# Kernel optimization log

Measured on AMD Instinct MI355X. Metric: run time of the kernel, lower is better.

The kernel has to match this reference:

```python
import jax, jax.numpy as jnp
import numpy as np

NUM_BLOCKS = 2
RES_LAYERS = 10
HID = 128
IN_CH = 256
MID_CH = 512
OUT_CH = 256
DILATIONS = [2 ** l for b in range(NUM_BLOCKS) for l in range(RES_LAYERS)]
GOOD = sum(DILATIONS)  # 2046
NLAYERS = NUM_BLOCKS * RES_LAYERS


def setup_inputs() -> dict:
    key = jax.random.key(0)
    ks = jax.random.split(key, 16)
    s = 0.05
    B, T = 8, 8192
    inp = {
        "inputs": jax.random.normal(ks[0], (B, IN_CH, T), dtype=jnp.float32),
        "Wi": jax.random.normal(ks[1], (HID, IN_CH), dtype=jnp.float32) * s,
        "bi": jax.random.normal(ks[2], (HID,), dtype=jnp.float32) * s,
        "Wf": jax.random.normal(ks[3], (NLAYERS, HID, HID, 2), dtype=jnp.float32) * s,
        "bf": jax.random.normal(ks[4], (NLAYERS, HID), dtype=jnp.float32) * s,
        "Wg": jax.random.normal(ks[5], (NLAYERS, HID, HID, 2), dtype=jnp.float32) * s,
        "bg": jax.random.normal(ks[6], (NLAYERS, HID), dtype=jnp.float32) * s,
        "Wr": jax.random.normal(ks[7], (NLAYERS, HID, HID), dtype=jnp.float32) * s,
        "br": jax.random.normal(ks[8], (NLAYERS, HID), dtype=jnp.float32) * s,
        "W1": jax.random.normal(ks[9], (MID_CH, HID), dtype=jnp.float32) * s,
        "b1": jax.random.normal(ks[10], (MID_CH,), dtype=jnp.float32) * s,
        "W2": jax.random.normal(ks[11], (OUT_CH, MID_CH), dtype=jnp.float32) * s,
        "b2": jax.random.normal(ks[12], (OUT_CH,), dtype=jnp.float32) * s,
    }
    return inp


def _dilated_k2(x, W, b, d):
    # x: [B, C, T] -> [B, C, T-d]
    y = jnp.einsum("oi,bit->bot", W[:, :, 0], x[:, :, :-d]) \
        + jnp.einsum("oi,bit->bot", W[:, :, 1], x[:, :, d:])
    return y + b[None, :, None]


def reference(inputs, Wi, bi, Wf, bf, Wg, bg, Wr, br, W1, b1, W2, b2):
    T = inputs.shape[2]
    target = T - GOOD
    res = jnp.einsum("oi,bit->bot", Wi, inputs) + bi[None, :, None]
    final = None
    for idx, d in enumerate(DILATIONS):
        f = jnp.tanh(_dilated_k2(res, Wf[idx], bf[idx], d))
        g = jax.nn.sigmoid(_dilated_k2(res, Wg[idx], bg[idx], d))
        out = f * g
        x = jnp.einsum("oi,bit->bot", Wr[idx], out) + br[idx][None, :, None]
        res = x + res[:, :, d:]
        # NOTE: original code computes split conv then immediately overwrites
        # it with x[:, :, -target:]; the split conv is dead code, so skip it.
        skip = x[:, :, -target:]
        final = skip if final is None else final + skip
    h = jax.nn.relu(final)
    h = jnp.einsum("oi,bit->bot", W1, h) + b1[None, :, None]
    h = jax.nn.relu(h)
    h = jnp.einsum("oi,bit->bot", W2, h) + b2[None, :, None]
    n, c, l = h.shape
    return jnp.transpose(h, (0, 2, 1)).reshape(n * l, c)
```

## Files before the change

kernel.cpp:

```cpp
#include <hip/hip_runtime.h>


#define TT 8192
#define HIDC 128
#define GOODC 2046
#define TGT 6146
#define NL 20

typedef _Float16 half8_t __attribute__((ext_vector_type(8)));
typedef _Float16 half4_t __attribute__((ext_vector_type(4)));
typedef float floatx4 __attribute__((ext_vector_type(4)));

__device__ __forceinline__ floatx4 mfma16(half8_t a, half8_t b, floatx4 c) {
  return __builtin_amdgcn_mfma_f32_16x16x32_f16(a, b, c, 0, 0, 0);
}

__global__ void prep_kernel(const float* __restrict__ Wi, const float* __restrict__ Wf,
                            const float* __restrict__ Wg, const float* __restrict__ Wr,
                            const float* __restrict__ W1, const float* __restrict__ W2,
                            _Float16* __restrict__ WIh, _Float16* __restrict__ WFG,
                            _Float16* __restrict__ WRh, _Float16* __restrict__ W1h,
                            _Float16* __restrict__ W2h) {
  int idx = blockIdx.x * blockDim.x + threadIdx.x;
  int stride = gridDim.x * blockDim.x;
  for (int i = idx; i < NL * 256 * 256; i += stride) {
    int l = i >> 16; int m = (i >> 8) & 255; int k = i & 255;
    int tap = k >> 7; int ci = k & 127;
    float v;
    if (m < 128) v = Wf[(((size_t)l * 128 + m) * 128 + ci) * 2 + tap];
    else         v = Wg[(((size_t)l * 128 + (m - 128)) * 128 + ci) * 2 + tap];
    WFG[i] = (_Float16)v;
  }
  for (int i = idx; i < NL * 128 * 128; i += stride) WRh[i] = (_Float16)Wr[i];
  for (int i = idx; i < 128 * 256; i += stride) WIh[i] = (_Float16)Wi[i];
  for (int i = idx; i < 512 * 128; i += stride) W1h[i] = (_Float16)W1[i];
  for (int i = idx; i < 256 * 512; i += stride) W2h[i] = (_Float16)W2[i];
}

__global__ __launch_bounds__(256, 3) void input_kernel(
    const float* __restrict__ inp, const _Float16* __restrict__ WIh,
    const float* __restrict__ bi, _Float16* __restrict__ R0) {
  __shared__ __align__(16) _Float16 Xs[64][264];
  const int tid = threadIdx.x;
  const int lane = tid & 63;
  const int w = tid >> 6;
  const int ml = lane & 15;
  const int mq = lane >> 4;
  const int b = blockIdx.y;
  const int u0 = blockIdx.x * 64;
  const float* ib = inp + (size_t)b * 256 * TT;

  for (int i = tid; i < 64 * 16; i += 256) {
    int n4 = i & 15;
    int kg = i >> 4;
    const float* src = ib + (size_t)(kg * 4) * TT + u0 + n4 * 4;
    floatx4 c0 = *(const floatx4*)(src);
    floatx4 c1 = *(const floatx4*)(src + TT);
    floatx4 c2 = *(const floatx4*)(src + 2 * TT);
    floatx4 c3 = *(const floatx4*)(src + 3 * TT);
#pragma unroll
    for (int t = 0; t < 4; ++t) {
      half4_t h;
      h[0] = (_Float16)c0[t]; h[1] = (_Float16)c1[t];
      h[2] = (_Float16)c2[t]; h[3] = (_Float16)c3[t];
      *(half4_t*)&Xs[n4 * 4 + t][kg * 4] = h;
    }
  }
  __syncthreads();

  floatx4 acc[2][4];
#pragma unroll
  for (int a = 0; a < 2; ++a)
#pragma unroll
    for (int c = 0; c < 4; ++c) acc[a][c] = floatx4{0.f, 0.f, 0.f, 0.f};

  const _Float16* Aw = WIh + (size_t)(32 * w + ml) * 256;
  for (int kk = 0; kk < 8; ++kk) {
    const int ko = kk * 32 + mq * 8;
    half8_t a0 = *(const half8_t*)(Aw + ko);
    half8_t a1 = *(const half8_t*)(Aw + 16 * 256 + ko);
#pragma unroll
    for (int nt = 0; nt < 4; ++nt) {
      half8_t bv = *(const half8_t*)&Xs[nt * 16 + ml][ko];
      acc[0][nt] = mfma16(a0, bv, acc[0][nt]);
      acc[1][nt] = mfma16(a1, bv, acc[1][nt]);
    }
  }
  __syncthreads();
  float* Xf = (float*)&Xs[0][0];
#pragma unroll
  for (int mt = 0; mt < 2; ++mt) {
    const int mb = 32 * w + mt * 16 + mq * 4;
#pragma unroll
    for (int nt = 0; nt < 4; ++nt)
      *(floatx4*)&Xf[(nt * 16 + ml) * 132 + mb] = acc[mt][nt];
  }
  __syncthreads();
  _Float16* Rb = R0 + (size_t)b * TT * HIDC;
  for (int i = tid; i < 64 * 16; i += 256) {
    int n = i >> 4; int c = i & 15;
    floatx4 x0 = *(const floatx4*)&Xf[n * 132 + c * 8];
    floatx4 x1 = *(const floatx4*)&Xf[n * 132 + c * 8 + 4];
    floatx4 b0 = *(const floatx4*)(bi + c * 8);
    floatx4 b1v = *(const floatx4*)(bi + c * 8 + 4);
    half8_t h;
#pragma unroll
    for (int t = 0; t < 4; ++t) {
      h[t] = (_Float16)(x0[t] + b0[t]);
      h[4 + t] = (_Float16)(x1[t] + b1v[t]);
    }
    *(half8_t*)(Rb + (size_t)(u0 + n) * HIDC + c * 8) = h;
  }
}

__global__ __launch_bounds__(512, 4) void layer_kernel(
    const _Float16* __restrict__ Rin, _Float16* __restrict__ Rout,
    const _Float16* __restrict__ WFG, const _Float16* __restrict__ WR,
    const float* __restrict__ bf, const float* __restrict__ bg,
    const float* __restrict__ br, int d, int ustart) {
  __shared__ __align__(16) _Float16 Xs[128][136];
  __shared__ __align__(16) _Float16 Os[128][136];
  const int tid = threadIdx.x;
  const int lane = tid & 63;
  const int w = tid >> 6;
  const int wm = w & 3;
  const int wn = w >> 2;
  const int ml = lane & 15;
  const int mq = lane >> 4;
  const int b = blockIdx.y;
  const int u0 = ustart + blockIdx.x * 128;
  const _Float16* Rb = Rin + (size_t)b * TT * HIDC;
  _Float16* Ro = Rout + (size_t)b * TT * HIDC;

  floatx4 accF[2][4], accG[2][4];
#pragma unroll
  for (int a = 0; a < 2; ++a)
#pragma unroll
    for (int c = 0; c < 4; ++c) {
      accF[a][c] = floatx4{0.f, 0.f, 0.f, 0.f};
      accG[a][c] = floatx4{0.f, 0.f, 0.f, 0.f};
    }

  for (int p = 0; p < 2; ++p) {
    for (int i = tid; i < 128 * 16; i += 512) {
      int n = i >> 4; int c = i & 15;
      int u = u0 + n - (p ? 0 : d);
      if (u > TT - 1) u = TT - 1;
      *(half8_t*)&Xs[n][c * 8] = *(const half8_t*)(Rb + (size_t)u * HIDC + c * 8);
    }
    __syncthreads();
    const _Float16* Af = WFG + (size_t)(32 * wm + ml) * 256 + p * 128;
    const _Float16* Ag = WFG + (size_t)(128 + 32 * wm + ml) * 256 + p * 128;
    for (int kk = 0; kk < 4; ++kk) {
      const int ko = kk * 32 + mq * 8;
      half8_t aF0 = *(const half8_t*)(Af + ko);
      half8_t aF1 = *(const half8_t*)(Af + 16 * 256 + ko);
      half8_t aG0 = *(const half8_t*)(Ag + ko);
      half8_t aG1 = *(const half8_t*)(Ag + 16 * 256 + ko);
#pragma unroll
      for (int nt = 0; nt < 4; ++nt) {
        half8_t bv = *(const half8_t*)&Xs[wn * 64 + nt * 16 + ml][ko];
        accF[0][nt] = mfma16(aF0, bv, accF[0][nt]);
        accF[1][nt] = mfma16(aF1, bv, accF[1][nt]);
        accG[0][nt] = mfma16(aG0, bv, accG[0][nt]);
        accG[1][nt] = mfma16(aG1, bv, accG[1][nt]);
      }
    }
    __syncthreads();
  }

#pragma unroll
  for (int mt = 0; mt < 2; ++mt) {
    const int mb = 32 * wm + mt * 16 + mq * 4;
    floatx4 bfv = *(const floatx4*)(bf + mb);
    floatx4 bgv = *(const floatx4*)(bg + mb);
#pragma unroll
    for (int nt = 0; nt < 4; ++nt) {
      half4_t o;
#pragma unroll
      for (int r = 0; r < 4; ++r) {
        float fp = accF[mt][nt][r] + bfv[r];
        float gp = accG[mt][nt][r] + bgv[r];
        float fv = 2.0f / (1.0f + __expf(-2.0f * fp)) - 1.0f;
        float gv = 1.0f / (1.0f + __expf(-gp));
        o[r] = (_Float16)(fv * gv);
      }
      *(half4_t*)&Os[wn * 64 + nt * 16 + ml][mb] = o;
    }
  }
  __syncthreads();

  floatx4 accX[2][4];
#pragma unroll
  for (int a = 0; a < 2; ++a)
#pragma unroll
    for (int c = 0; c < 4; ++c) accX[a][c] = floatx4{0.f, 0.f, 0.f, 0.f};
  const _Float16* Ar = WR + (size_t)(32 * wm + ml) * 128;
#pragma unroll
  for (int kk = 0; kk < 4; ++kk) {
    const int ko = kk * 32 + mq * 8;
    half8_t a0 = *(const half8_t*)(Ar + ko);
    half8_t a1 = *(const half8_t*)(Ar + 16 * 128 + ko);
#pragma unroll
    for (int nt = 0; nt < 4; ++nt) {
      half8_t bv = *(const half8_t*)&Os[wn * 64 + nt * 16 + ml][ko];
      accX[0][nt] = mfma16(a0, bv, accX[0][nt]);
      accX[1][nt] = mfma16(a1, bv, accX[1][nt]);
    }
  }
  __syncthreads();

#pragma unroll
  for (int mt = 0; mt < 2; ++mt) {
    const int mb = 32 * wm + mt * 16 + mq * 4;
#pragma unroll
    for (int nt = 0; nt < 4; ++nt) {
      half4_t h;
#pragma unroll
      for (int r = 0; r < 4; ++r) h[r] = (_Float16)accX[mt][nt][r];
      *(half4_t*)&Os[wn * 64 + nt * 16 + ml][mb] = h;
    }
  }
  __syncthreads();

  for (int i = tid; i < 128 * 16; i += 512) {
    int n = i >> 4; int c = i & 15;
    int u = u0 + n;
    if (u < TT) {
      half8_t xv = *(const half8_t*)&Os[n][c * 8];
      half8_t rv = *(const half8_t*)&Xs[n][c * 8];
      floatx4 b0 = *(const floatx4*)(br + c * 8);
      floatx4 b1v = *(const floatx4*)(br + c * 8 + 4);
      half8_t o;
#pragma unroll
      for (int t = 0; t < 4; ++t) {
        o[t] = (_Float16)((float)xv[t] + (float)rv[t] + b0[t]);
        o[4 + t] = (_Float16)((float)xv[4 + t] + (float)rv[4 + t] + b1v[t]);
      }
      *(half8_t*)(Ro + (size_t)u * HIDC + c * 8) = o;
    }
  }
}

__global__ __launch_bounds__(512, 4) void head_kernel(
    const _Float16* __restrict__ Rfin, const _Float16* __restrict__ R0,
    const _Float16* __restrict__ W1h, const _Float16* __restrict__ W2h,
    const float* __restrict__ b1, const float* __restrict__ b2,
    float* __restrict__ out) {
  __shared__ __align__(16) _Float16 Hs[64][136];
  __shared__ __align__(16) _Float16 H1s[64][264];
  const int tid = threadIdx.x;
  const int lane = tid & 63;
  const int w = tid >> 6;
  const int ml = lane & 15;
  const int mq = lane >> 4;
  const int b = blockIdx.y;
  const int u0 = GOODC + blockIdx.x * 64;
  const _Float16* Ra = Rfin + (size_t)b * TT * HIDC;
  const _Float16* Rz = R0 + (size_t)b * TT * HIDC;

  for (int i = tid; i < 64 * 16; i += 512) {
    int n = i >> 4; int c = i & 15;
    int u = u0 + n; if (u > TT - 1) u = TT - 1;
    half8_t a = *(const half8_t*)(Ra + (size_t)u * HIDC + c * 8);
    half8_t z = *(const half8_t*)(Rz + (size_t)u * HIDC + c * 8);
    half8_t h;
#pragma unroll
    for (int t = 0; t < 8; ++t) {
      float v = (float)a[t] - (float)z[t];
      h[t] = (_Float16)(v > 0.f ? v : 0.f);
    }
    *(half8_t*)&Hs[n][c * 8] = h;
  }
  __syncthreads();

  floatx4 acc2[2][4];
#pragma unroll
  for (int a = 0; a < 2; ++a)
#pragma unroll
    for (int c = 0; c < 4; ++c) acc2[a][c] = floatx4{0.f, 0.f, 0.f, 0.f};

  for (int p = 0; p < 2; ++p) {
    floatx4 acc1[2][4];
#pragma unroll
    for (int a = 0; a < 2; ++a)
#pragma unroll
      for (int c = 0; c < 4; ++c) acc1[a][c] = floatx4{0.f, 0.f, 0.f, 0.f};
    const _Float16* A1 = W1h + (size_t)(256 * p + 32 * w + ml) * 128;
#pragma unroll
    for (int kk = 0; kk < 4; ++kk) {
      const int ko = kk * 32 + mq * 8;
      half8_t av0 = *(const half8_t*)(A1 + ko);
      half8_t av1 = *(const half8_t*)(A1 + 16 * 128 + ko);
#pragma unroll
      for (int nt = 0; nt < 4; ++nt) {
        half8_t bv = *(const half8_t*)&Hs[nt * 16 + ml][ko];
        acc1[0][nt] = mfma16(av0, bv, acc1[0][nt]);
        acc1[1][nt] = mfma16(av1, bv, acc1[1][nt]);
      }
    }
    __syncthreads();
#pragma unroll
    for (int mt = 0; mt < 2; ++mt) {
      const int mb = 32 * w + mt * 16 + mq * 4;
      floatx4 bv = *(const floatx4*)(b1 + 256 * p + mb);
#pragma unroll
      for (int nt = 0; nt < 4; ++nt) {
        half4_t h;
#pragma unroll
        for (int r = 0; r < 4; ++r) {
          float v = acc1[mt][nt][r] + bv[r];
          h[r] = (_Float16)(v > 0.f ? v : 0.f);
        }
        *(half4_t*)&H1s[nt * 16 + ml][mb] = h;
      }
    }
    __syncthreads();
    const _Float16* A2 = W2h + (size_t)(32 * w + ml) * 512 + p * 256;
    for (int kk = 0; kk < 8; ++kk) {
      const int ko = kk * 32 + mq * 8;
      half8_t av0 = *(const half8_t*)(A2 + ko);
      half8_t av1 = *(const half8_t*)(A2 + 16 * 512 + ko);
#pragma unroll
      for (int nt = 0; nt < 4; ++nt) {
        half8_t bv = *(const half8_t*)&H1s[nt * 16 + ml][ko];
        acc2[0][nt] = mfma16(av0, bv, acc2[0][nt]);
        acc2[1][nt] = mfma16(av1, bv, acc2[1][nt]);
      }
    }
    __syncthreads();
  }

#pragma unroll
  for (int mt = 0; mt < 2; ++mt) {
    const int mb = 32 * w + mt * 16 + mq * 4;
    floatx4 bv = *(const floatx4*)(b2 + mb);
#pragma unroll
    for (int nt = 0; nt < 4; ++nt) {
      half4_t h;
#pragma unroll
      for (int r = 0; r < 4; ++r) h[r] = (_Float16)(acc2[mt][nt][r] + bv[r]);
      *(half4_t*)&H1s[nt * 16 + ml][mb] = h;
    }
  }
  __syncthreads();
  for (int i = tid; i < 64 * 32; i += 512) {
    int n = i >> 5; int g = i & 31;
    int u = u0 + n;
    if (u < TT) {
      half8_t v = *(const half8_t*)&H1s[n][g * 8];
      float* dst = out + ((size_t)b * TGT + (u - GOODC)) * 256 + g * 8;
      floatx4 v0, v1;
#pragma unroll
      for (int t = 0; t < 4; ++t) { v0[t] = (float)v[t]; v1[t] = (float)v[4 + t]; }
      *(floatx4*)dst = v0;
      *(floatx4*)(dst + 4) = v1;
    }
  }
}

extern "C" void kernel_launch(void* const* d_in, const int* in_sizes, int n_in,
                              void* d_out, int out_size, void* d_ws, size_t ws_size,
                              hipStream_t stream) {
  const float* inputs = (const float*)d_in[0];
  const float* Wi = (const float*)d_in[1];
  const float* bi = (const float*)d_in[2];
  const float* Wf = (const float*)d_in[3];
  const float* bf = (const float*)d_in[4];
  const float* Wg = (const float*)d_in[5];
  const float* bg = (const float*)d_in[6];
  const float* Wr = (const float*)d_in[7];
  const float* br = (const float*)d_in[8];
  const float* W1 = (const float*)d_in[9];
  const float* b1 = (const float*)d_in[10];
  const float* W2 = (const float*)d_in[11];
  const float* b2 = (const float*)d_in[12];
  float* out = (float*)d_out;

  char* ws = (char*)d_ws;
  _Float16* R0h = (_Float16*)(ws + 0);
  _Float16* Ph  = (_Float16*)(ws + 16777216);
  _Float16* Qh  = (_Float16*)(ws + 33554432);
  _Float16* WFG = (_Float16*)(ws + 50331648);
  _Float16* WRh = (_Float16*)(ws + 52953088);
  _Float16* WIh = (_Float16*)(ws + 53608448);
  _Float16* W1h = (_Float16*)(ws + 53673984);
  _Float16* W2h = (_Float16*)(ws + 53805056);

  prep_kernel<<<dim3(512), dim3(256), 0, stream>>>(Wi, Wf, Wg, Wr, W1, W2,
                                                   WIh, WFG, WRh, W1h, W2h);
  input_kernel<<<dim3(TT / 64, 8), dim3(256), 0, stream>>>(inputs, WIh, bi, R0h);

  int S = 0;
  for (int l = 0; l < NL; ++l) {
    int d = 1 << (l % 10);
    int ustart = S + d;
    const _Float16* rin = (l == 0) ? R0h : ((l & 1) ? Ph : Qh);
    _Float16* rout = (l & 1) ? Qh : Ph;
    int Lout = TT - ustart;
    int nblk = (Lout + 127) / 128;
    layer_kernel<<<dim3(nblk, 8), dim3(512), 0, stream>>>(
        rin, rout, WFG + (size_t)l * 65536, WRh + (size_t)l * 16384,
        bf + l * 128, bg + l * 128, br + l * 128, d, ustart);
    S = ustart;
  }
  head_kernel<<<dim3((TGT + 63) / 64, 8), dim3(512), 0, stream>>>(
      Qh, R0h, W1h, W2h, b1, b2, out);
}
```

Measured before the change: 857.5 us.

## Restructure layer and head kernels with async LDS loads, swizzle, and fused epilogues

The layer kernel now loads both conv taps at once into a 96-row swizzled LDS tile using global_load_lds. This removes the two-pass load/sync loop. It also writes the residual output straight from the accumulators, dropping the LDS round trip and two barriers, and uses rcp-based tanh/sigmoid. A fixed grid of 86 blocks aligned at position 0 is launched, and blocks below ustart exit early. The head kernel is retiled to 128 columns, with output accumulators held across the four mid-channel chunks and fp32 results stored directly. This raises register pressure and changes load coalescing.

```diff
diff --git a/kernel.cpp b/kernel.cpp
--- a/kernel.cpp
+++ b/kernel.cpp
@@ -13,6 +13,19 @@
 
 __device__ __forceinline__ floatx4 mfma16(half8_t a, half8_t b, floatx4 c) {
   return __builtin_amdgcn_mfma_f32_16x16x32_f16(a, b, c, 0, 0, 0);
+}
+
+__device__ __forceinline__ void gload_lds16(const _Float16* g, _Float16* l) {
+  __builtin_amdgcn_global_load_lds(
+      (const __attribute__((address_space(1))) unsigned int*)(const void*)g,
+      (__attribute__((address_space(3))) unsigned int*)(void*)l, 16, 0, 0);
+}
+
+__device__ __forceinline__ float fast_sigmoid(float x) {
+  return __builtin_amdgcn_rcpf(1.0f + __expf(-x));
+}
+__device__ __forceinline__ float fast_tanh(float x) {
+  return 2.0f * __builtin_amdgcn_rcpf(1.0f + __expf(-2.0f * x)) - 1.0f;
 }
 
 __global__ void prep_kernel(const float* __restrict__ Wi, const float* __restrict__ Wf,
@@ -118,8 +131,8 @@
     const _Float16* __restrict__ WFG, const _Float16* __restrict__ WR,
     const float* __restrict__ bf, const float* __restrict__ bg,
     const float* __restrict__ br, int d, int ustart) {
-  __shared__ __align__(16) _Float16 Xs[128][136];
-  __shared__ __align__(16) _Float16 Os[128][136];
+  __shared__ __align__(16) _Float16 Xs[96 * 256];
+  __shared__ __align__(16) _Float16 Os[96][136];
   const int tid = threadIdx.x;
   const int lane = tid & 63;
   const int w = tid >> 6;
@@ -128,45 +141,51 @@
   const int ml = lane & 15;
   const int mq = lane >> 4;
   const int b = blockIdx.y;
-  const int u0 = ustart + blockIdx.x * 128;
+  const int u0 = blockIdx.x * 96;
+  if (u0 + 95 < ustart) return;
   const _Float16* Rb = Rin + (size_t)b * TT * HIDC;
   _Float16* Ro = Rout + (size_t)b * TT * HIDC;
 
-  floatx4 accF[2][4], accG[2][4];
+#pragma unroll
+  for (int it = 0; it < 6; ++it) {
+    int chunk = (w * 6 + it) * 64 + lane;
+    int n = chunk >> 5;
+    int pg = chunk & 31;
+    int lg = pg ^ (n & 7);
+    int tap = lg >> 4;
+    int c8 = (lg & 15) << 3;
+    int u = u0 + n - (tap ? 0 : d);
+    u = min(max(u, 0), TT - 1);
+    gload_lds16(Rb + (size_t)u * HIDC + c8, &Xs[(w * 6 + it) * 512]);
+  }
+  __syncthreads();
+
+  floatx4 accF[2][3], accG[2][3];
 #pragma unroll
   for (int a = 0; a < 2; ++a)
 #pragma unroll
-    for (int c = 0; c < 4; ++c) {
+    for (int c = 0; c < 3; ++c) {
       accF[a][c] = floatx4{0.f, 0.f, 0.f, 0.f};
       accG[a][c] = floatx4{0.f, 0.f, 0.f, 0.f};
     }
-
-  for (int p = 0; p < 2; ++p) {
-    for (int i = tid; i < 128 * 16; i += 512) {
-      int n = i >> 4; int c = i & 15;
-      int u = u0 + n - (p ? 0 : d);
-      if (u > TT - 1) u = TT - 1;
-      *(half8_t*)&Xs[n][c * 8] = *(const half8_t*)(Rb + (size_t)u * HIDC + c * 8);
-    }
-    __syncthreads();
-    const _Float16* Af = WFG + (size_t)(32 * wm + ml) * 256 + p * 128;
-    const _Float16* Ag = WFG + (size_t)(128 + 32 * wm + ml) * 256 + p * 128;
-    for (int kk = 0; kk < 4; ++kk) {
-      const int ko = kk * 32 + mq * 8;
-      half8_t aF0 = *(const half8_t*)(Af + ko);
-      half8_t aF1 = *(const half8_t*)(Af + 16 * 256 + ko);
-      half8_t aG0 = *(const half8_t*)(Ag + ko);
-      half8_t aG1 = *(const half8_t*)(Ag + 16 * 256 + ko);
-#pragma unroll
-      for (int nt = 0; nt < 4; ++nt) {
-        half8_t bv = *(const half8_t*)&Xs[wn * 64 + nt * 16 + ml][ko];
-        accF[0][nt] = mfma16(aF0, bv, accF[0][nt]);
-        accF[1][nt] = mfma16(aF1, bv, accF[1][nt]);
-        accG[0][nt] = mfma16(aG0, bv, accG[0][nt]);
-        accG[1][nt] = mfma16(aG1, bv, accG[1][nt]);
-      }
-    }
-    __syncthreads();
+  const _Float16* Af = WFG + (size_t)(32 * wm + ml) * 256;
+  const _Float16* Ag = Af + 128 * 256;
+  for (int kk = 0; kk < 8; ++kk) {
+    const int ko = kk * 32 + mq * 8;
+    const int g = ko >> 3;
+    half8_t aF0 = *(const half8_t*)(Af + ko);
+    half8_t aF1 = *(const half8_t*)(Af + 16 * 256 + ko);
+    half8_t aG0 = *(const half8_t*)(Ag + ko);
+    half8_t aG1 = *(const half8_t*)(Ag + 16 * 256 + ko);
+#pragma unroll
+    for (int nt = 0; nt < 3; ++nt) {
+      const int row = wn * 48 + nt * 16 + ml;
+      half8_t bv = *(const half8_t*)&Xs[row * 256 + ((g ^ (row & 7)) << 3)];
+      accF[0][nt] = mfma16(aF0, bv, accF[0][nt]);
+      accF[1][nt] = mfma16(aF1, bv, accF[1][nt]);
+      accG[0][nt] = mfma16(aG0, bv, accG[0][nt]);
+      accG[1][nt] = mfma16(aG1, bv, accG[1][nt]);
+    }
   }
 
 #pragma unroll
@@ -175,26 +194,24 @@
     floatx4 bfv = *(const floatx4*)(bf + mb);
     floatx4 bgv = *(const floatx4*)(bg + mb);
 #pragma unroll
-    for (int nt = 0; nt < 4; ++nt) {
+    for (int nt = 0; nt < 3; ++nt) {
       half4_t o;
 #pragma unroll
       for (int r = 0; r < 4; ++r) {
-        float fp = accF[mt][nt][r] + bfv[r];
-        float gp = accG[mt][nt][r] + bgv[r];
-        float fv = 2.0f / (1.0f + __expf(-2.0f * fp)) - 1.0f;
-        float gv = 1.0f / (1.0f + __expf(-gp));
+        float fv = fast_tanh(accF[mt][nt][r] + bfv[r]);
+        float gv = fast_sigmoid(accG[mt][nt][r] + bgv[r]);
         o[r] = (_Float16)(fv * gv);
       }
-      *(half4_t*)&Os[wn * 64 + nt * 16 + ml][mb] = o;
-    }
-  }
-  __syncthreads();
-
-  floatx4 accX[2][4];
+      *(half4_t*)&Os[wn * 48 + nt * 16 + ml][mb] = o;
+    }
+  }
+  __syncthreads();
+
+  floatx4 accX[2][3];
 #pragma unroll
   for (int a = 0; a < 2; ++a)
 #pragma unroll
-    for (int c = 0; c < 4; ++c) accX[a][c] = floatx4{0.f, 0.f, 0.f, 0.f};
+    for (int c = 0; c < 3; ++c) accX[a][c] = floatx4{0.f, 0.f, 0.f, 0.f};
   const _Float16* Ar = WR + (size_t)(32 * wm + ml) * 128;
 #pragma unroll
   for (int kk = 0; kk < 4; ++kk) {
@@ -202,42 +219,31 @@
     half8_t a0 = *(const half8_t*)(Ar + ko);
     half8_t a1 = *(const half8_t*)(Ar + 16 * 128 + ko);
 #pragma unroll
-    for (int nt = 0; nt < 4; ++nt) {
-      half8_t bv = *(const half8_t*)&Os[wn * 64 + nt * 16 + ml][ko];
+    for (int nt = 0; nt < 3; ++nt) {
+      half8_t bv = *(const half8_t*)&Os[wn * 48 + nt * 16 + ml][ko];
       accX[0][nt] = mfma16(a0, bv, accX[0][nt]);
       accX[1][nt] = mfma16(a1, bv, accX[1][nt]);
     }
   }
-  __syncthreads();
 
 #pragma unroll
   for (int mt = 0; mt < 2; ++mt) {
     const int mb = 32 * wm + mt * 16 + mq * 4;
-#pragma unroll
-    for (int nt = 0; nt < 4; ++nt) {
-      half4_t h;
-#pragma unroll
-      for (int r = 0; r < 4; ++r) h[r] = (_Float16)accX[mt][nt][r];
-      *(half4_t*)&Os[wn * 64 + nt * 16 + ml][mb] = h;
-    }
-  }
-  __syncthreads();
-
-  for (int i = tid; i < 128 * 16; i += 512) {
-    int n = i >> 4; int c = i & 15;
-    int u = u0 + n;
-    if (u < TT) {
-      half8_t xv = *(const half8_t*)&Os[n][c * 8];
-      half8_t rv = *(const half8_t*)&Xs[n][c * 8];
-      floatx4 b0 = *(const floatx4*)(br + c * 8);
-      floatx4 b1v = *(const floatx4*)(br + c * 8 + 4);
-      half8_t o;
-#pragma unroll
-      for (int t = 0; t < 4; ++t) {
-        o[t] = (_Float16)((float)xv[t] + (float)rv[t] + b0[t]);
-        o[4 + t] = (_Float16)((float)xv[4 + t] + (float)rv[4 + t] + b1v[t]);
-      }
-      *(half8_t*)(Ro + (size_t)u * HIDC + c * 8) = o;
+    floatx4 brv = *(const floatx4*)(br + mb);
+    const int lgT = 16 + (mb >> 3);
+    const int off = mb & 7;
+#pragma unroll
+    for (int nt = 0; nt < 3; ++nt) {
+      const int n = wn * 48 + nt * 16 + ml;
+      const int u = u0 + n;
+      if (u >= ustart && u < TT) {
+        half4_t rold = *(const half4_t*)&Xs[n * 256 + ((lgT ^ (n & 7)) << 3) + off];
+        half4_t o;
+#pragma unroll
+        for (int r = 0; r < 4; ++r)
+          o[r] = (_Float16)(accX[mt][nt][r] + brv[r] + (float)rold[r]);
+        *(half4_t*)(Ro + (size_t)u * HIDC + mb) = o;
+      }
     }
   }
 }
@@ -247,19 +253,21 @@
     const _Float16* __restrict__ W1h, const _Float16* __restrict__ W2h,
     const float* __restrict__ b1, const float* __restrict__ b2,
     float* __restrict__ out) {
-  __shared__ __align__(16) _Float16 Hs[64][136];
-  __shared__ __align__(16) _Float16 H1s[64][264];
+  __shared__ __align__(16) _Float16 Hs[128][136];
+  __shared__ __align__(16) _Float16 H1s[128][136];
   const int tid = threadIdx.x;
   const int lane = tid & 63;
   const int w = tid >> 6;
+  const int mg = w & 3;
+  const int ng = w >> 2;
   const int ml = lane & 15;
   const int mq = lane >> 4;
   const int b = blockIdx.y;
-  const int u0 = GOODC + blockIdx.x * 64;
+  const int u0 = GOODC + blockIdx.x * 128;
   const _Float16* Ra = Rfin + (size_t)b * TT * HIDC;
   const _Float16* Rz = R0 + (size_t)b * TT * HIDC;
 
-  for (int i = tid; i < 64 * 16; i += 512) {
+  for (int i = tid; i < 128 * 16; i += 512) {
     int n = i >> 4; int c = i & 15;
     int u = u0 + n; if (u > TT - 1) u = TT - 1;
     half8_t a = *(const half8_t*)(Ra + (size_t)u * HIDC + c * 8);
@@ -274,19 +282,19 @@
   }
   __syncthreads();
 
-  floatx4 acc2[2][4];
-#pragma unroll
-  for (int a = 0; a < 2; ++a)
-#pragma unroll
-    for (int c = 0; c < 4; ++c) acc2[a][c] = floatx4{0.f, 0.f, 0.f, 0.f};
-
-  for (int p = 0; p < 2; ++p) {
+  floatx4 accO[4][4];
+#pragma unroll
+  for (int a = 0; a < 4; ++a)
+#pragma unroll
+    for (int c = 0; c < 4; ++c) accO[a][c] = floatx4{0.f, 0.f, 0.f, 0.f};
+
+  for (int p = 0; p < 4; ++p) {
     floatx4 acc1[2][4];
 #pragma unroll
     for (int a = 0; a < 2; ++a)
 #pragma unroll
       for (int c = 0; c < 4; ++c) acc1[a][c] = floatx4{0.f, 0.f, 0.f, 0.f};
-    const _Float16* A1 = W1h + (size_t)(256 * p + 32 * w + ml) * 128;
+    const _Float16* A1 = W1h + (size_t)(128 * p + 32 * mg + ml) * 128;
 #pragma unroll
     for (int kk = 0; kk < 4; ++kk) {
       const int ko = kk * 32 + mq * 8;
@@ -294,7 +302,7 @@
       half8_t av1 = *(const half8_t*)(A1 + 16 * 128 + ko);
 #pragma unroll
       for (int nt = 0; nt < 4; ++nt) {
-        half8_t bv = *(const half8_t*)&Hs[nt * 16 + ml][ko];
+        half8_t bv = *(const half8_t*)&Hs[ng * 64 + nt * 16 + ml][ko];
         acc1[0][nt] = mfma16(av0, bv, acc1[0][nt]);
         acc1[1][nt] = mfma16(av1, bv, acc1[1][nt]);
       }
@@ -302,8 +310,8 @@
     __syncthreads();
 #pragma unroll
     for (int mt = 0; mt < 2; ++mt) {
-      const int mb = 32 * w + mt * 16 + mq * 4;
-      floatx4 bv = *(const floatx4*)(b1 + 256 * p + mb);
+      const int kc = 32 * mg + mt * 16 + mq * 4;
+      floatx4 bv = *(const floatx4*)(b1 + 128 * p + kc);
 #pragma unroll
       for (int nt = 0; nt < 4; ++nt) {
         half4_t h;
@@ -312,49 +320,37 @@
           float v = acc1[mt][nt][r] + bv[r];
           h[r] = (_Float16)(v > 0.f ? v : 0.f);
         }
-        *(half4_t*)&H1s[nt * 16 + ml][mb] = h;
+        *(half4_t*)&H1s[ng * 64 + nt * 16 + ml][kc] = h;
       }
     }
     __syncthreads();
-    const _Float16* A2 = W2h + (size_t)(32 * w + ml) * 512 + p * 256;
-    for (int kk = 0; kk < 8; ++kk) {
+    const _Float16* A2 = W2h + (size_t)(64 * mg + ml) * 512 + p * 128;
+#pragma unroll
+    for (int kk = 0; kk < 4; ++kk) {
       const int ko = kk * 32 + mq * 8;
-      half8_t av0 = *(const half8_t*)(A2 + ko);
-      half8_t av1 = *(const half8_t*)(A2 + 16 * 512 + ko);
 #pragma unroll
       for (int nt = 0; nt < 4; ++nt) {
-        half8_t bv = *(const half8_t*)&H1s[nt * 16 + ml][ko];
-        acc2[0][nt] = mfma16(av0, bv, acc2[0][nt]);
-        acc2[1][nt] = mfma16(av1, bv, acc2[1][nt]);
-      }
-    }
-    __syncthreads();
-  }
-
-#pragma unroll
-  for (int mt = 0; mt < 2; ++mt) {
-    const int mb = 32 * w + mt * 16 + mq * 4;
-    floatx4 bv = *(const floatx4*)(b2 + mb);
+        half8_t bv = *(const half8_t*)&H1s[ng * 64 + nt * 16 + ml][ko];
+#pragma unroll
+        for (int mt = 0; mt < 4; ++mt) {
+          half8_t av = *(const half8_t*)(A2 + (size_t)(mt * 16) * 512 + ko);
+          accO[mt][nt] = mfma16(av, bv, accO[mt][nt]);
+        }
+      }
+    }
+  }
+
+#pragma unroll
+  for (int mt = 0; mt < 4; ++mt) {
+    const int m = 64 * mg + mt * 16 + mq * 4;
+    floatx4 b2v = *(const floatx4*)(b2 + m);
 #pragma unroll
     for (int nt = 0; nt < 4; ++nt) {
-      half4_t h;
-#pragma unroll
-      for (int r = 0; r < 4; ++r) h[r] = (_Float16)(acc2[mt][nt][r] + bv[r]);
-      *(half4_t*)&H1s[nt * 16 + ml][mb] = h;
-    }
-  }
-  __syncthreads();
-  for (int i = tid; i < 64 * 32; i += 512) {
-    int n = i >> 5; int g = i & 31;
-    int u = u0 + n;
-    if (u < TT) {
-      half8_t v = *(const half8_t*)&H1s[n][g * 8];
-      float* dst = out + ((size_t)b * TGT + (u - GOODC)) * 256 + g * 8;
-      floatx4 v0, v1;
-#pragma unroll
-      for (int t = 0; t < 4; ++t) { v0[t] = (float)v[t]; v1[t] = (float)v[4 + t]; }
-      *(floatx4*)dst = v0;
-      *(floatx4*)(dst + 4) = v1;
+      const int n = ng * 64 + nt * 16 + ml;
+      const int u = u0 + n;
+      if (u < TT) {
+        *(floatx4*)(out + ((size_t)b * TGT + (u - GOODC)) * 256 + m) = accO[mt][nt] + b2v;
+      }
     }
   }
 }
@@ -397,13 +393,11 @@
     int ustart = S + d;
     const _Float16* rin = (l == 0) ? R0h : ((l & 1) ? Ph : Qh);
     _Float16* rout = (l & 1) ? Qh : Ph;
-    int Lout = TT - ustart;
-    int nblk = (Lout + 127) / 128;
-    layer_kernel<<<dim3(nblk, 8), dim3(512), 0, stream>>>(
+    layer_kernel<<<dim3(86, 8), dim3(512), 0, stream>>>(
         rin, rout, WFG + (size_t)l * 65536, WRh + (size_t)l * 16384,
         bf + l * 128, bg + l * 128, br + l * 128, d, ustart);
     S = ustart;
   }
-  head_kernel<<<dim3((TGT + 63) / 64, 8), dim3(512), 0, stream>>>(
+  head_kernel<<<dim3((TGT + 127) / 128, 8), dim3(512), 0, stream>>>(
       Qh, R0h, W1h, W2h, b1, b2, out);
 }
```

New measurement: 1.028 ms. 19.8% more time.
